# Performance work log

Hardware: AMD Instinct MI355X
Metric: run time of the kernel (lower is better)

Reference implementation:

```python
import jax, jax.numpy as jnp
import numpy as np

B, S, D = 1, 2048, 2048
H = 32          # num_heads == num_kv_heads (n_rep = 1)
QB = 8          # rosa_num_query_key_bits
VB = 8          # rosa_num_value_bits
TAU = 1.0


def setup_inputs() -> dict:
    key = jax.random.key(0)
    ks = jax.random.split(key, 8)
    s = 0.02
    return {
        "hidden_states": jax.random.normal(ks[0], (B, S, D), dtype=jnp.float32),
        "Wq": jax.random.normal(ks[1], (D, H * QB), dtype=jnp.float32) * s,
        "Wk": jax.random.normal(ks[2], (D, H * QB), dtype=jnp.float32) * s,
        "Wv": jax.random.normal(ks[3], (D, H * VB), dtype=jnp.float32) * s,
        "Wo": jax.random.normal(ks[4], (H * VB, D), dtype=jnp.float32) * s,
        "Wg": jax.random.normal(ks[5], (D, D), dtype=jnp.float32) * s,
        "v_emb0": jnp.full((H * VB,), -1e-05, dtype=jnp.float32),
        "v_emb1": jnp.full((H * VB,), +1e-05, dtype=jnp.float32),
    }


def _rosa_attention(hs, Wq, Wk, Wv, Wo, Wg, v_emb0, v_emb1):
    b, s, _ = hs.shape
    # low-bit projections -> [B, H, S, bits]
    q = (hs @ Wq).reshape(b, s, H, QB).transpose(0, 2, 1, 3)
    k = (hs @ Wk).reshape(b, s, H, QB).transpose(0, 2, 1, 3)
    v = (hs @ Wv).reshape(b, s, H, VB).transpose(0, 2, 1, 3)
    # soft-binarized bit probabilities (training-mode relaxation, temperature tau)
    pq = jax.nn.sigmoid(q / TAU)
    pk = jax.nn.sigmoid(k / TAU)
    pv = jax.nn.sigmoid(v / TAU)
    # expected number of matching bits:
    # sum_d pq*pk + (1-pq)*(1-pk) = 2*<pq,pk> - sum(pq) - sum(pk) + QB
    dot = jnp.einsum('bhqd,bhkd->bhqk', pq, pk)
    scores = 2.0 * dot - pq.sum(-1)[..., :, None] - pk.sum(-1)[..., None, :] + QB
    # causal mask
    causal = jnp.tril(jnp.ones((s, s), dtype=bool))
    scores = jnp.where(causal, scores / TAU, jnp.finfo(scores.dtype).min)
    attn = jax.nn.softmax(scores, axis=-1)
    out = jnp.einsum('bhqk,bhkd->bhqd', attn, pv)           # [B,H,S,VB], in (0,1)
    out = out.transpose(0, 2, 1, 3).reshape(b, s, H * VB)
    # binary value-embedding interpolation
    out = v_emb1 * out + v_emb0 * (1.0 - out)
    out = out @ Wo
    gate = jax.nn.sigmoid(hs @ Wg)
    return out * gate


def reference(hidden_states, Wq, Wk, Wv, Wo, Wg, v_emb0, v_emb1):
    return _rosa_attention(hidden_states, Wq, Wk, Wv, Wo, Wg, v_emb0, v_emb1)
```

## Files before the change

kernel.cpp:

```cpp
#include <hip/hip_runtime.h>

#define S 2048
#define DIM 2048
#define H 32
#define NB 2816
#define SA 25.0f
#define SW 1150.0f

using u16 = unsigned short;
using u8 = unsigned char;
using short8 = __attribute__((ext_vector_type(8))) short;
using f32x4 = __attribute__((ext_vector_type(4))) float;
using i32x4 = __attribute__((ext_vector_type(4))) int;

__device__ __forceinline__ u16 f2bf(float x) {
  union { float f; unsigned u; } v; v.f = x;
  unsigned r = v.u + 0x7fffu + ((v.u >> 16) & 1u);
  return (u16)(r >> 16);
}
__device__ __forceinline__ int clampi(int x) { return x < -127 ? -127 : (x > 127 ? 127 : x); }
__device__ __forceinline__ unsigned q4i8(float a, float b, float c, float d, float s) {
  int x0 = clampi((int)rintf(a * s)), x1 = clampi((int)rintf(b * s));
  int x2 = clampi((int)rintf(c * s)), x3 = clampi((int)rintf(d * s));
  return (x0 & 255) | ((x1 & 255) << 8) | ((x2 & 255) << 16) | ((unsigned)(x3 & 255) << 24);
}

#define GLOAD_LDS16(g, l)                                                      \
  __builtin_amdgcn_global_load_lds(                                            \
      (const __attribute__((address_space(1))) unsigned*)(g),                  \
      (__attribute__((address_space(3))) unsigned*)(l), 16, 0, 0)

__global__ __launch_bounds__(256)
void trans_all_k(const float* __restrict__ Wq, const float* __restrict__ Wk,
                 const float* __restrict__ Wv, const float* __restrict__ Wg,
                 const float* __restrict__ Wo, const float* __restrict__ hs,
                 u16* __restrict__ Wt, u8* __restrict__ Wg8, u16* __restrict__ Wot,
                 u16* __restrict__ Abf, u8* __restrict__ A8) {
  int b = blockIdx.x;
  const int t = threadIdx.x;
  if (b >= 1536) {
    int i = ((b - 1536) * 256 + t) * 8;
    float4 a = *(const float4*)(hs + i);
    float4 c = *(const float4*)(hs + i + 4);
    uint4 r;
    r.x = f2bf(a.x) | ((unsigned)f2bf(a.y) << 16);
    r.y = f2bf(a.z) | ((unsigned)f2bf(a.w) << 16);
    r.z = f2bf(c.x) | ((unsigned)f2bf(c.y) << 16);
    r.w = f2bf(c.z) | ((unsigned)f2bf(c.w) << 16);
    int row = i >> 11, k = i & 2047;
    int dst = (row << 11) + (k & ~63) + ((((k >> 3) & 7) ^ (row & 7)) << 3);
    *(uint4*)(Abf + dst) = r;
    uint2 q;
    q.x = q4i8(a.x, a.y, a.z, a.w, SA);
    q.y = q4i8(c.x, c.y, c.z, c.w, SA);
    int dst8 = (row << 11) + (k & ~63) + ((((k >> 4) & 3) ^ (row & 3)) << 4) + (k & 8);
    *(uint2*)(A8 + dst8) = q;
    return;
  }
  const float* in; int K, N;
  int mode;
  u16* out = nullptr;
  if (b < 384) {
    K = 2048; N = 256; mode = 0;
    in = (b < 128) ? Wq : (b < 256) ? Wk : Wv;
    out = Wt + (size_t)(b >> 7) * 256 * 2048;
    b &= 127;
  } else if (b < 1408) {
    in = Wg; mode = 1; K = 2048; N = 2048; b -= 384;
  } else {
    in = Wo; out = Wot; mode = 2; K = 256; N = 2048; b -= 1408;
  }
  const int nbN = N >> 6;
  const int kb = (b / nbN) << 6, nb = (b % nbN) << 6;
  __shared__ float tile[64][65];
  const int n4 = (t & 15) * 4;
#pragma unroll
  for (int p = 0; p < 4; p++) {
    int k = p * 16 + (t >> 4);
    float4 v = *(const float4*)(in + (size_t)(kb + k) * N + nb + n4);
    tile[k][n4] = v.x; tile[k][n4 + 1] = v.y; tile[k][n4 + 2] = v.z; tile[k][n4 + 3] = v.w;
  }
  __syncthreads();
  const int k8 = (t & 7) * 8;
#pragma unroll
  for (int p = 0; p < 2; p++) {
    int n = p * 32 + (t >> 3);
    if (mode == 1) {
      int nr = nb + n;
      uint2 w;
      w.x = q4i8(tile[k8 + 0][n], tile[k8 + 1][n], tile[k8 + 2][n], tile[k8 + 3][n], SW);
      w.y = q4i8(tile[k8 + 4][n], tile[k8 + 5][n], tile[k8 + 6][n], tile[k8 + 7][n], SW);
      int col = kb + ((((k8 >> 4) ^ (nr & 3))) << 4) + (k8 & 8);
      *(uint2*)(Wg8 + (size_t)nr * 2048 + col) = w;
    } else {
      uint4 w;
      w.x = f2bf(tile[k8 + 0][n]) | ((unsigned)f2bf(tile[k8 + 1][n]) << 16);
      w.y = f2bf(tile[k8 + 2][n]) | ((unsigned)f2bf(tile[k8 + 3][n]) << 16);
      w.z = f2bf(tile[k8 + 4][n]) | ((unsigned)f2bf(tile[k8 + 5][n]) << 16);
      w.w = f2bf(tile[k8 + 6][n]) | ((unsigned)f2bf(tile[k8 + 7][n]) << 16);
      if (mode == 2) {
        *(uint4*)(out + (size_t)(nb + n) * K + kb + k8) = w;
      } else {
        int nr = nb + n;
        int col = kb + ((((k8 >> 3) ^ (nr & 7))) << 3);
        *(uint4*)(out + (size_t)nr * 2048 + col) = w;
      }
    }
  }
}

__global__ __launch_bounds__(256)
void gemm1_mix_k(const u16* __restrict__ Abf, const u16* __restrict__ Wt,
                 const u8* __restrict__ A8, const u8* __restrict__ Wg8,
                 float* __restrict__ C) {
  __shared__ __align__(16) char smem[65536];
  const int t = threadIdx.x;
  const int bn = blockIdx.x, bm = blockIdx.y * 128;
  const int wave = t >> 6, lane = t & 63;
  const int wm = (wave >> 1) * 64, wn = (wave & 1) * 64;
  const int l16 = lane & 15, quad = lane >> 4;
  const int K = 2048;
  const int srow = t >> 3;
  if (bn < 6) {
    typedef u16 (*Tile)[128][64];
    Tile As = (Tile)smem;
    Tile Bs = (Tile)(smem + 32768);
    const int scol = (t & 7) * 8;
    const u16* Ap = Abf + (size_t)(bm + srow) * K + scol;
    const u16* Bp = Wt + (size_t)(bn * 128 + srow) * K + scol;
#define STAGE1(buf, koff)                                                      \
  do {                                                                         \
    GLOAD_LDS16(Ap + (koff), &As[buf][srow][scol]);                            \
    GLOAD_LDS16(Ap + 32 * (size_t)K + (koff), &As[buf][srow + 32][scol]);      \
    GLOAD_LDS16(Ap + 64 * (size_t)K + (koff), &As[buf][srow + 64][scol]);      \
    GLOAD_LDS16(Ap + 96 * (size_t)K + (koff), &As[buf][srow + 96][scol]);      \
    GLOAD_LDS16(Bp + (koff), &Bs[buf][srow][scol]);                            \
    GLOAD_LDS16(Bp + 32 * (size_t)K + (koff), &Bs[buf][srow + 32][scol]);      \
    GLOAD_LDS16(Bp + 64 * (size_t)K + (koff), &Bs[buf][srow + 64][scol]);      \
    GLOAD_LDS16(Bp + 96 * (size_t)K + (koff), &Bs[buf][srow + 96][scol]);      \
  } while (0)
    f32x4 acc[4][4];
#pragma unroll
    for (int i = 0; i < 4; i++)
#pragma unroll
      for (int j = 0; j < 4; j++) acc[i][j] = (f32x4){0.f, 0.f, 0.f, 0.f};
    STAGE1(0, 0);
    for (int kk = 0; kk < K; kk += 64) {
      const int cur = (kk >> 6) & 1, nxt = cur ^ 1;
      __syncthreads();
      if (kk + 64 < K) STAGE1(nxt, kk + 64);
      short8 af[4][2], bf[4][2];
#pragma unroll
      for (int mt = 0; mt < 4; mt++) {
        int row = wm + mt * 16 + l16;
        int rs = (row & 7) << 3;
        af[mt][0] = *(const short8*)&As[cur][row][(quad << 3) ^ rs];
        af[mt][1] = *(const short8*)&As[cur][row][((quad + 4) << 3) ^ rs];
      }
#pragma unroll
      for (int nt = 0; nt < 4; nt++) {
        int row = wn + nt * 16 + l16;
        int rs = (row & 7) << 3;
        bf[nt][0] = *(const short8*)&Bs[cur][row][(quad << 3) ^ rs];
        bf[nt][1] = *(const short8*)&Bs[cur][row][((quad + 4) << 3) ^ rs];
      }
#pragma unroll
      for (int mt = 0; mt < 4; mt++)
#pragma unroll
        for (int nt = 0; nt < 4; nt++) {
          acc[mt][nt] = __builtin_amdgcn_mfma_f32_16x16x32_bf16(af[mt][0], bf[nt][0], acc[mt][nt], 0, 0, 0);
          acc[mt][nt] = __builtin_amdgcn_mfma_f32_16x16x32_bf16(af[mt][1], bf[nt][1], acc[mt][nt], 0, 0, 0);
        }
    }
#pragma unroll
    for (int mt = 0; mt < 4; mt++)
#pragma unroll
      for (int nt = 0; nt < 4; nt++)
#pragma unroll
        for (int r = 0; r < 4; r++) {
          int m = bm + wm + mt * 16 + quad * 4 + r;
          int n = bn * 128 + wn + nt * 16 + l16;
          float v = acc[mt][nt][r];
          C[(size_t)m * NB + n] = 1.f / (1.f + __expf(-v));
        }
#undef STAGE1
  } else {
    typedef u8 (*TileG)[128][128];
    TileG As = (TileG)smem;
    TileG Bs = (TileG)(smem + 32768);
    const int scol = (t & 7) * 16;
    const u8* Ap = A8 + (size_t)(bm + srow) * K + scol;
    const u8* Bp = Wg8 + (size_t)((bn - 6) * 128 + srow) * K + scol;
#define STAGEG(buf, koff)                                                      \
  do {                                                                         \
    GLOAD_LDS16(Ap + (koff), &As[buf][srow][scol]);                            \
    GLOAD_LDS16(Ap + 32 * (size_t)K + (koff), &As[buf][srow + 32][scol]);      \
    GLOAD_LDS16(Ap + 64 * (size_t)K + (koff), &As[buf][srow + 64][scol]);      \
    GLOAD_LDS16(Ap + 96 * (size_t)K + (koff), &As[buf][srow + 96][scol]);      \
    GLOAD_LDS16(Bp + (koff), &Bs[buf][srow][scol]);                            \
    GLOAD_LDS16(Bp + 32 * (size_t)K + (koff), &Bs[buf][srow + 32][scol]);      \
    GLOAD_LDS16(Bp + 64 * (size_t)K + (koff), &Bs[buf][srow + 64][scol]);      \
    GLOAD_LDS16(Bp + 96 * (size_t)K + (koff), &Bs[buf][srow + 96][scol]);      \
  } while (0)
    i32x4 acc[4][4];
#pragma unroll
    for (int i = 0; i < 4; i++)
#pragma unroll
      for (int j = 0; j < 4; j++) acc[i][j] = (i32x4){0, 0, 0, 0};
    STAGEG(0, 0);
    for (int kk = 0; kk < K; kk += 128) {
      const int cur = (kk >> 7) & 1, nxt = cur ^ 1;
      __syncthreads();
      if (kk + 128 < K) STAGEG(nxt, kk + 128);
      i32x4 af[4][2], bf[4][2];
#pragma unroll
      for (int mt = 0; mt < 4; mt++) {
        int row = wm + mt * 16 + l16;
        int sl = (quad ^ (row & 3)) << 4;
        af[mt][0] = *(const i32x4*)&As[cur][row][sl];
        af[mt][1] = *(const i32x4*)&As[cur][row][64 + sl];
      }
#pragma unroll
      for (int nt = 0; nt < 4; nt++) {
        int row = wn + nt * 16 + l16;
        int sl = (quad ^ (row & 3)) << 4;
        bf[nt][0] = *(const i32x4*)&Bs[cur][row][sl];
        bf[nt][1] = *(const i32x4*)&Bs[cur][row][64 + sl];
      }
#pragma unroll
      for (int mt = 0; mt < 4; mt++)
#pragma unroll
        for (int nt = 0; nt < 4; nt++) {
          acc[mt][nt] = __builtin_amdgcn_mfma_i32_16x16x64_i8(af[mt][0], bf[nt][0], acc[mt][nt], 0, 0, 0);
          acc[mt][nt] = __builtin_amdgcn_mfma_i32_16x16x64_i8(af[mt][1], bf[nt][1], acc[mt][nt], 0, 0, 0);
        }
    }
    const float inv = 1.f / (SA * SW);
#pragma unroll
    for (int mt = 0; mt < 4; mt++)
#pragma unroll
      for (int nt = 0; nt < 4; nt++)
#pragma unroll
        for (int r = 0; r < 4; r++) {
          int m = bm + wm + mt * 16 + quad * 4 + r;
          int n = bn * 128 + wn + nt * 16 + l16;
          float v = (float)acc[mt][nt][r] * inv;
          C[(size_t)m * NB + n] = 1.f / (1.f + __expf(-v));
        }
#undef STAGEG
  }
}

__global__ __launch_bounds__(256)
void gemm64_k(const u16* __restrict__ A, const u16* __restrict__ Bt,
              float* __restrict__ C, const float* __restrict__ gate,
              int K, int ldc) {
  __shared__ u16 As[2][64][32];
  __shared__ u16 Bs[2][64][32];
  const int t = threadIdx.x;
  const int bm = blockIdx.y * 64, bn = blockIdx.x * 64;
  const int wave = t >> 6, lane = t & 63;
  const int wm = (wave >> 1) * 32, wn = (wave & 1) * 32;
  const int l16 = lane & 15, quad = lane >> 4;
  const int srow = t >> 2, scol = (t & 3) * 8;
  const u16* Ap = A + (size_t)(bm + srow) * K + scol;
  const u16* Bp = Bt + (size_t)(bn + srow) * K + scol;
  f32x4 acc[2][2];
#pragma unroll
  for (int i = 0; i < 2; i++)
#pragma unroll
    for (int j = 0; j < 2; j++) acc[i][j] = (f32x4){0.f, 0.f, 0.f, 0.f};
  GLOAD_LDS16(Ap, &As[0][srow][scol]);
  GLOAD_LDS16(Bp, &Bs[0][srow][scol]);
  for (int kk = 0; kk < K; kk += 32) {
    const int cur = (kk >> 5) & 1, nxt = cur ^ 1;
    __syncthreads();
    if (kk + 32 < K) {
      GLOAD_LDS16(Ap + kk + 32, &As[nxt][srow][scol]);
      GLOAD_LDS16(Bp + kk + 32, &Bs[nxt][srow][scol]);
    }
    short8 af[2], bf[2];
#pragma unroll
    for (int mt = 0; mt < 2; mt++) af[mt] = *(const short8*)&As[cur][wm + mt * 16 + l16][quad * 8];
#pragma unroll
    for (int nt = 0; nt < 2; nt++) bf[nt] = *(const short8*)&Bs[cur][wn + nt * 16 + l16][quad * 8];
#pragma unroll
    for (int mt = 0; mt < 2; mt++)
#pragma unroll
      for (int nt = 0; nt < 2; nt++)
        acc[mt][nt] = __builtin_amdgcn_mfma_f32_16x16x32_bf16(af[mt], bf[nt], acc[mt][nt], 0, 0, 0);
  }
#pragma unroll
  for (int mt = 0; mt < 2; mt++)
#pragma unroll
    for (int nt = 0; nt < 2; nt++)
#pragma unroll
      for (int r = 0; r < 4; r++) {
        int m = bm + wm + mt * 16 + quad * 4 + r;
        int n = bn + wn + nt * 16 + l16;
        float v = acc[mt][nt][r] * gate[(size_t)m * NB + n];
        C[(size_t)m * ldc + n] = v;
      }
}

__global__ __launch_bounds__(256)
void attn_mfma_k(const float* __restrict__ P, float* __restrict__ Part) {
  __shared__ u16 Plds[128 * 128];
  __shared__ u16 Vt[16 * 264];
  __shared__ u16 Klds[256 * 8];
  __shared__ u16 Qlds[128 * 8];
  __shared__ float sk2[256];
  const int h = blockIdx.y;
  int tau = blockIdx.x, m = 0;
  while (tau >= (m >> 1) + 1) { tau -= (m >> 1) + 1; m++; }
  const int kc = tau;
  const bool needMask = (kc == (m >> 1));
  const int q0 = m * 128, kb = kc * 256;
  const int t = threadIdx.x, wave = t >> 6, lane = t & 63;
  const int l16 = lane & 15, quad = lane >> 4;
  if (t < 128) {
    const float* rq = P + (size_t)(q0 + t) * NB + h * 8;
    float4 a = *(const float4*)rq, b = *(const float4*)(rq + 4);
    uint4 w;
    w.x = f2bf(a.x) | ((unsigned)f2bf(a.y) << 16);
    w.y = f2bf(a.z) | ((unsigned)f2bf(a.w) << 16);
    w.z = f2bf(b.x) | ((unsigned)f2bf(b.y) << 16);
    w.w = f2bf(b.z) | ((unsigned)f2bf(b.w) << 16);
    *(uint4*)&Qlds[t * 8] = w;
  }
  {
    const float* rk = P + (size_t)(kb + t) * NB + 256 + h * 8;
    float4 k0 = *(const float4*)rk, k1 = *(const float4*)(rk + 4);
    float4 v0 = *(const float4*)(rk + 256), v1 = *(const float4*)(rk + 260);
    sk2[t] = (k0.x + k0.y + k0.z + k0.w + k1.x + k1.y + k1.z + k1.w) * 1.44269504f;
    uint4 w;
    w.x = f2bf(k0.x) | ((unsigned)f2bf(k0.y) << 16);
    w.y = f2bf(k0.z) | ((unsigned)f2bf(k0.w) << 16);
    w.z = f2bf(k1.x) | ((unsigned)f2bf(k1.y) << 16);
    w.w = f2bf(k1.z) | ((unsigned)f2bf(k1.w) << 16);
    *(uint4*)&Klds[t * 8] = w;
    Vt[0 * 264 + t] = f2bf(v0.x); Vt[1 * 264 + t] = f2bf(v0.y);
    Vt[2 * 264 + t] = f2bf(v0.z); Vt[3 * 264 + t] = f2bf(v0.w);
    Vt[4 * 264 + t] = f2bf(v1.x); Vt[5 * 264 + t] = f2bf(v1.y);
    Vt[6 * 264 + t] = f2bf(v1.z); Vt[7 * 264 + t] = f2bf(v1.w);
    Vt[8 * 264 + t] = 0x3F80;
#pragma unroll
    for (int d = 9; d < 16; d++) Vt[d * 264 + t] = 0;
  }
  __syncthreads();
  short8 bq[2];
#pragma unroll
  for (int i = 0; i < 2; i++) {
    short8 z = {0, 0, 0, 0, 0, 0, 0, 0};
    if (quad == 0) z = *(const short8*)&Qlds[((wave * 2 + i) * 16 + l16) * 8];
    bq[i] = z;
  }
  f32x4 O[2];
  O[0] = (f32x4){0.f, 0.f, 0.f, 0.f};
  O[1] = (f32x4){0.f, 0.f, 0.f, 0.f};
  const int nsl = needMask ? (m & 1) + 1 : 2;
  const int swz = (l16 >> 1) & 7;
  for (int sl = 0; sl < nsl; sl++) {
    const int ks = sl * 128;
    const bool dm = needMask && (sl == (m & 1));
    for (int kt = 0; kt < 8; kt++) {
      short8 ak = {0, 0, 0, 0, 0, 0, 0, 0};
      if (quad == 0) ak = *(const short8*)&Klds[(ks + kt * 16 + l16) * 8];
      float4 s2 = *(const float4*)&sk2[ks + kt * 16 + quad * 4];
#pragma unroll
      for (int i = 0; i < 2; i++) {
        f32x4 c = __builtin_amdgcn_mfma_f32_16x16x32_bf16(
            ak, bq[i], (f32x4){0.f, 0.f, 0.f, 0.f}, 0, 0, 0);
        float e0 = exp2f(c[0] * 2.88539008f - s2.x);
        float e1 = exp2f(c[1] * 2.88539008f - s2.y);
        float e2 = exp2f(c[2] * 2.88539008f - s2.z);
        float e3 = exp2f(c[3] * 2.88539008f - s2.w);
        if (dm) {
          int q = q0 + (wave * 2 + i) * 16 + l16;
          int key = kb + ks + kt * 16 + quad * 4;
          e0 = (key + 0 <= q) ? e0 : 0.f;
          e1 = (key + 1 <= q) ? e1 : 0.f;
          e2 = (key + 2 <= q) ? e2 : 0.f;
          e3 = (key + 3 <= q) ? e3 : 0.f;
        }
        uint2 pk2;
        pk2.x = f2bf(e0) | ((unsigned)f2bf(e1) << 16);
        pk2.y = f2bf(e2) | ((unsigned)f2bf(e3) << 16);
        int row = (wave * 2 + i) * 16 + l16;
        int cb = 2 * kt + (quad >> 1);
        int pb = cb ^ swz;
        *(uint2*)&Plds[row * 128 + pb * 8 + (quad & 1) * 4] = pk2;
      }
    }
#pragma unroll
    for (int kc4 = 0; kc4 < 4; kc4++) {
      short8 bv = *(const short8*)&Vt[l16 * 264 + ks + kc4 * 32 + quad * 8];
#pragma unroll
      for (int i = 0; i < 2; i++) {
        int row = (wave * 2 + i) * 16 + l16;
        int pb = (kc4 * 4 + quad) ^ swz;
        short8 ap = *(const short8*)&Plds[row * 128 + pb * 8];
        O[i] = __builtin_amdgcn_mfma_f32_16x16x32_bf16(ap, bv, O[i], 0, 0, 0);
      }
    }
  }
  if (l16 < 9) {
#pragma unroll
    for (int i = 0; i < 2; i++) {
      int qb = q0 + (wave * 2 + i) * 16 + quad * 4;
#pragma unroll
      for (int r = 0; r < 4; r++)
        Part[(((size_t)h * S + qb + r) * 8 + kc) * 12 + l16] = O[i][r];
    }
  }
}

__global__ __launch_bounds__(256)
void attn_merge_k(const float* __restrict__ Part, const float* __restrict__ e0,
                  const float* __restrict__ e1, u16* __restrict__ O2) {
  const int q = blockIdx.x;
  const int t = threadIdx.x;
  const int d = t & 7;
  const int nch = (q >> 8) + 1;
  size_t base = ((size_t)(t >> 3) * S + q) * 8 * 12;
  float ov = 0.f, lv = 0.f;
  for (int kc = 0; kc < nch; kc++) {
    ov += Part[base + (size_t)kc * 12 + d];
    lv += Part[base + (size_t)kc * 12 + 8];
  }
  float outv = ov / lv;
  float r = e0[t] + (e1[t] - e0[t]) * outv;
  O2[(size_t)q * 256 + t] = f2bf(r);
}

extern "C" void kernel_launch(void* const* d_in, const int* in_sizes, int n_in,
                              void* d_out, int out_size, void* d_ws, size_t ws_size,
                              hipStream_t stream) {
  const float* hs = (const float*)d_in[0];
  const float* Wq = (const float*)d_in[1];
  const float* Wk = (const float*)d_in[2];
  const float* Wv = (const float*)d_in[3];
  const float* Wo = (const float*)d_in[4];
  const float* Wg = (const float*)d_in[5];
  const float* e0 = (const float*)d_in[6];
  const float* e1 = (const float*)d_in[7];
  float* out = (float*)d_out;
  char* ws = (char*)d_ws;
  u16*   Abf  = (u16*)(ws + 0);
  u8*    A8   = (u8*)(ws + 8388608);
  u16*   Wt   = (u16*)(ws + 12582912);
  u8*    Wg8  = (u8*)(ws + 15728640);
  u16*   Wot  = (u16*)(ws + 19922944);
  u16*   O2   = (u16*)(ws + 20971520);
  float* P    = (float*)(ws + 22020096);
  float* Part = (float*)(ws + 45088768);

  trans_all_k<<<dim3(3584), 256, 0, stream>>>(Wq, Wk, Wv, Wg, Wo, hs, Wt, Wg8, Wot, Abf, A8);
  gemm1_mix_k<<<dim3(22, 16), 256, 0, stream>>>(Abf, Wt, A8, Wg8, P);
  attn_mfma_k<<<dim3(72, H), 256, 0, stream>>>(P, Part);
  attn_merge_k<<<dim3(S), 256, 0, stream>>>(Part, e0, e1, O2);
  gemm64_k<<<dim3(DIM / 64, S / 64), 256, 0, stream>>>(O2, Wot, out, P + 768, 256, DIM);
}
```

Baseline: 174.6 us.

## Pre-pack projection weights into MFMA fragment layout and load B directly to registers

The bf16 projection weights are now written by the prep kernel in a fragment-major layout of 16 rows by 32 k-elements, so each lane can load its MFMA B operand straight from global memory. The A tile is still staged through LDS, while the B tile no longer uses LDS at all. The k-loop is unrolled by two, with register double buffering for B. This is meant to halve LDS traffic and LDS stores for the QKV projection. In exchange it adds register pressure and relies on global/L2 latency for the B fragments.

```diff
diff --git a/kernel.cpp b/kernel.cpp
--- a/kernel.cpp
+++ b/kernel.cpp
@@ -102,8 +102,8 @@
         *(uint4*)(out + (size_t)(nb + n) * K + kb + k8) = w;
       } else {
         int nr = nb + n;
-        int col = kb + ((((k8 >> 3) ^ (nr & 7))) << 3);
-        *(uint4*)(out + (size_t)nr * 2048 + col) = w;
+        size_t frag = ((size_t)(nr >> 4)) * 64 + ((kb + k8) >> 5);
+        *(uint4*)(out + frag * 512 + (nr & 15) * 32 + (k8 & 31)) = w;
       }
     }
   }
@@ -122,55 +122,69 @@
   const int K = 2048;
   const int srow = t >> 3;
   if (bn < 6) {
-    typedef u16 (*Tile)[128][64];
-    Tile As = (Tile)smem;
-    Tile Bs = (Tile)(smem + 32768);
+    typedef u16 (*TileA)[128][64];
+    TileA As = (TileA)smem;
     const int scol = (t & 7) * 8;
     const u16* Ap = Abf + (size_t)(bm + srow) * K + scol;
-    const u16* Bp = Wt + (size_t)(bn * 128 + srow) * K + scol;
-#define STAGE1(buf, koff)                                                      \
+    const int cb = bn * 8 + (wn >> 4);
+    const int lelem = l16 * 32 + quad * 8;
+#define STAGE_A(buf, koff)                                                     \
   do {                                                                         \
     GLOAD_LDS16(Ap + (koff), &As[buf][srow][scol]);                            \
     GLOAD_LDS16(Ap + 32 * (size_t)K + (koff), &As[buf][srow + 32][scol]);      \
     GLOAD_LDS16(Ap + 64 * (size_t)K + (koff), &As[buf][srow + 64][scol]);      \
     GLOAD_LDS16(Ap + 96 * (size_t)K + (koff), &As[buf][srow + 96][scol]);      \
-    GLOAD_LDS16(Bp + (koff), &Bs[buf][srow][scol]);                            \
-    GLOAD_LDS16(Bp + 32 * (size_t)K + (koff), &Bs[buf][srow + 32][scol]);      \
-    GLOAD_LDS16(Bp + 64 * (size_t)K + (koff), &Bs[buf][srow + 64][scol]);      \
-    GLOAD_LDS16(Bp + 96 * (size_t)K + (koff), &Bs[buf][srow + 96][scol]);      \
+  } while (0)
+#define LOAD_B(dst, kk)                                                        \
+  do {                                                                         \
+    _Pragma("unroll")                                                          \
+    for (int nt = 0; nt < 4; nt++) {                                           \
+      _Pragma("unroll")                                                        \
+      for (int h = 0; h < 2; h++)                                              \
+        dst[nt][h] = *(const short8*)&Wt[((size_t)(cb + nt) * 64 +             \
+                                          ((kk) >> 5) + h) * 512 + lelem];     \
+    }                                                                          \
+  } while (0)
+#define COMPUTE_BF(buf, B)                                                     \
+  do {                                                                         \
+    short8 af[4][2];                                                           \
+    _Pragma("unroll")                                                          \
+    for (int mt = 0; mt < 4; mt++) {                                           \
+      int row = wm + mt * 16 + l16;                                            \
+      int rs = (row & 7) << 3;                                                 \
+      af[mt][0] = *(const short8*)&As[buf][row][(quad << 3) ^ rs];             \
+      af[mt][1] = *(const short8*)&As[buf][row][((quad + 4) << 3) ^ rs];       \
+    }                                                                          \
+    _Pragma("unroll")                                                          \
+    for (int mt = 0; mt < 4; mt++) {                                           \
+      _Pragma("unroll")                                                        \
+      for (int nt = 0; nt < 4; nt++) {                                         \
+        acc[mt][nt] = __builtin_amdgcn_mfma_f32_16x16x32_bf16(                 \
+            af[mt][0], B[nt][0], acc[mt][nt], 0, 0, 0);                        \
+        acc[mt][nt] = __builtin_amdgcn_mfma_f32_16x16x32_bf16(                 \
+            af[mt][1], B[nt][1], acc[mt][nt], 0, 0, 0);                        \
+      }                                                                        \
+    }                                                                          \
   } while (0)
     f32x4 acc[4][4];
 #pragma unroll
     for (int i = 0; i < 4; i++)
 #pragma unroll
       for (int j = 0; j < 4; j++) acc[i][j] = (f32x4){0.f, 0.f, 0.f, 0.f};
-    STAGE1(0, 0);
-    for (int kk = 0; kk < K; kk += 64) {
-      const int cur = (kk >> 6) & 1, nxt = cur ^ 1;
+    short8 b0[4][2], b1[4][2];
+    LOAD_B(b0, 0);
+    STAGE_A(0, 0);
+    for (int kk = 0; kk < K; kk += 128) {
       __syncthreads();
-      if (kk + 64 < K) STAGE1(nxt, kk + 64);
-      short8 af[4][2], bf[4][2];
-#pragma unroll
-      for (int mt = 0; mt < 4; mt++) {
-        int row = wm + mt * 16 + l16;
-        int rs = (row & 7) << 3;
-        af[mt][0] = *(const short8*)&As[cur][row][(quad << 3) ^ rs];
-        af[mt][1] = *(const short8*)&As[cur][row][((quad + 4) << 3) ^ rs];
-      }
-#pragma unroll
-      for (int nt = 0; nt < 4; nt++) {
-        int row = wn + nt * 16 + l16;
-        int rs = (row & 7) << 3;
-        bf[nt][0] = *(const short8*)&Bs[cur][row][(quad << 3) ^ rs];
-        bf[nt][1] = *(const short8*)&Bs[cur][row][((quad + 4) << 3) ^ rs];
-      }
-#pragma unroll
-      for (int mt = 0; mt < 4; mt++)
-#pragma unroll
-        for (int nt = 0; nt < 4; nt++) {
-          acc[mt][nt] = __builtin_amdgcn_mfma_f32_16x16x32_bf16(af[mt][0], bf[nt][0], acc[mt][nt], 0, 0, 0);
-          acc[mt][nt] = __builtin_amdgcn_mfma_f32_16x16x32_bf16(af[mt][1], bf[nt][1], acc[mt][nt], 0, 0, 0);
-        }
+      STAGE_A(1, kk + 64);
+      LOAD_B(b1, kk + 64);
+      COMPUTE_BF(0, b0);
+      __syncthreads();
+      if (kk + 128 < K) {
+        STAGE_A(0, kk + 128);
+        LOAD_B(b0, kk + 128);
+      }
+      COMPUTE_BF(1, b1);
     }
 #pragma unroll
     for (int mt = 0; mt < 4; mt++)
@@ -183,7 +197,9 @@
           float v = acc[mt][nt][r];
           C[(size_t)m * NB + n] = 1.f / (1.f + __expf(-v));
         }
-#undef STAGE1
+#undef STAGE_A
+#undef LOAD_B
+#undef COMPUTE_BF
   } else {
     typedef u8 (*TileG)[128][128];
     TileG As = (TileG)smem;
```

New measurement: 185.1 us. 1.06x slower.
